# Kernel tuning notes

Measured on AMD Instinct MI355X. Metric: run time of the kernel, lower is better.

Reference implementation:

```python
import jax, jax.numpy as jnp
import numpy as np

D_MODEL = 1024
FEED = 4096
HEADS = 16
EPS = 1e-5


def _ln(x, g, b):
    mu = jnp.mean(x, axis=-1, keepdims=True)
    var = jnp.var(x, axis=-1, keepdims=True)
    return (x - mu) * jax.lax.rsqrt(var + EPS) * g + b


def setup_inputs() -> dict:
    key = jax.random.key(0)
    ks = jax.random.split(key, 8)
    s = 0.02
    return {
        "src": jax.random.normal(ks[0], (8, 512, D_MODEL), jnp.float32),
        "wq": jax.random.normal(ks[1], (D_MODEL, D_MODEL), jnp.float32) * s,
        "bq": jnp.zeros((D_MODEL,), jnp.float32),
        "wk": jax.random.normal(ks[2], (D_MODEL, D_MODEL), jnp.float32) * s,
        "bk": jnp.zeros((D_MODEL,), jnp.float32),
        "wv": jax.random.normal(ks[3], (D_MODEL, D_MODEL), jnp.float32) * s,
        "bv": jnp.zeros((D_MODEL,), jnp.float32),
        "g1": jnp.ones((D_MODEL,), jnp.float32),
        "be1": jnp.zeros((D_MODEL,), jnp.float32),
        "w1": jax.random.normal(ks[4], (D_MODEL, FEED), jnp.float32) * s,
        "b1": jnp.zeros((FEED,), jnp.float32),
        "w2": jax.random.normal(ks[5], (FEED, D_MODEL), jnp.float32) * s,
        "b2": jnp.zeros((D_MODEL,), jnp.float32),
        "g2": jnp.ones((D_MODEL,), jnp.float32),
        "be2": jnp.zeros((D_MODEL,), jnp.float32),
    }


def reference(src, wq, bq, wk, bk, wv, bv, g1, be1, w1, b1, w2, b2, g2, be2):
    bs, seq, d = src.shape
    dk = d // HEADS
    q = src @ wq + bq
    k = src @ wk + bk
    v = src @ wv + bv
    # [B, H, S, dk]
    q = q.reshape(bs, seq, HEADS, dk).transpose(0, 2, 1, 3)
    k = k.reshape(bs, seq, HEADS, dk).transpose(0, 2, 1, 3)
    v = v.reshape(bs, seq, HEADS, dk).transpose(0, 2, 1, 3)
    scores = jnp.einsum('bhqd,bhkd->bhqk', q, k)  # no mask (src_mask unused in original)
    att = jax.nn.softmax(scores / jnp.sqrt(jnp.float32(dk)), axis=-1)
    ctx = jnp.einsum('bhqk,bhkd->bhqd', att, v)
    ctx = ctx.transpose(0, 2, 1, 3).reshape(bs, seq, d)  # concat heads
    x = _ln(ctx + src, g1, be1)
    # FFN (dropout = identity at eval)
    h = jax.nn.relu(x @ w1 + b1)
    y = h @ w2 + b2
    return _ln(y + x, g2, be2)
```

## Files before the change

kernel.cpp:

```cpp
#include <hip/hip_runtime.h>
#include <hip/hip_bf16.h>
#include <stdint.h>

#define DM   1024
#define FF   4096
#define NH   16
#define DK   64
#define SEQ  512
#define NTOK 4096

typedef __attribute__((ext_vector_type(8))) unsigned short ushort8;
typedef __attribute__((ext_vector_type(4))) unsigned short ushort4v;
typedef __attribute__((ext_vector_type(8))) short bf16x8;
typedef __attribute__((ext_vector_type(4))) float f32x4;

__device__ __forceinline__ float bf2f(unsigned short u) {
  union { unsigned int i; float f; } v; v.i = ((unsigned int)u) << 16; return v.f;
}
__device__ __forceinline__ unsigned short f2bf(float f) {
  union { float fl; unsigned int i; } v; v.fl = f;
  v.i += 0x7fffu + ((v.i >> 16) & 1u);
  return (unsigned short)(v.i >> 16);
}

__device__ __forceinline__ void gload16(const unsigned short* g, unsigned short* l) {
  __builtin_amdgcn_global_load_lds(
      (const __attribute__((address_space(1))) unsigned int*)g,
      (__attribute__((address_space(3))) unsigned int*)l, 16, 0, 0);
}

__global__ __launch_bounds__(256)
void f32_to_bf16(const float* __restrict__ in, unsigned short* __restrict__ out,
                 long n) {
  long i = ((long)blockIdx.x * 256 + threadIdx.x) * 4;
  if (i + 3 < n) {
    f32x4 v = *(const f32x4*)(in + i);
    ushort4v o;
#pragma unroll
    for (int j = 0; j < 4; j++) o[j] = f2bf(v[j]);
    *(ushort4v*)(out + i) = o;
  }
}

__global__ void transpose_f2b(const float* __restrict__ in, int ldin,
                              unsigned short* __restrict__ out, int ldout) {
  __shared__ unsigned short tile[32][33];
  const int tx = threadIdx.x, ty = threadIdx.y;
  const long r0 = (long)blockIdx.y * 32, c0 = (long)blockIdx.x * 32;
#pragma unroll
  for (int i = 0; i < 4; i++)
    tile[ty + i * 8][tx] = f2bf(in[(r0 + ty + i * 8) * ldin + c0 + tx]);
  __syncthreads();
#pragma unroll
  for (int i = 0; i < 4; i++)
    out[(c0 + ty + i * 8) * ldout + r0 + tx] = tile[tx][ty + i * 8];
}

__global__ void transpose_v(const unsigned short* __restrict__ QKV,
                            unsigned short* __restrict__ Vt) {
  __shared__ unsigned short tile[32][33];
  const int tx = threadIdx.x, ty = threadIdx.y;
  const int bh = blockIdx.z, b = bh >> 4, h = bh & 15;
  const int s0 = blockIdx.y * 32, d0 = blockIdx.x * 32;
  const unsigned short* inb = QKV + (long)(b * SEQ) * 3072 + 2048 + h * 64;
#pragma unroll
  for (int i = 0; i < 4; i++)
    tile[ty + i * 8][tx] = inb[(long)(s0 + ty + i * 8) * 3072 + d0 + tx];
  __syncthreads();
#pragma unroll
  for (int i = 0; i < 4; i++)
    Vt[(long)bh * (DK * SEQ) + (long)(d0 + ty + i * 8) * SEQ + s0 + tx] =
        tile[tx][ty + i * 8];
}

__global__ void concat3(const float* __restrict__ a, const float* __restrict__ b,
                        const float* __restrict__ c, float* __restrict__ o) {
  int i = blockIdx.x * 256 + threadIdx.x;
  if (i < 3072)
    o[i] = (i < 1024) ? a[i] : ((i < 2048) ? b[i - 1024] : c[i - 2048]);
}

template <bool RELU, bool PARTIAL>
__global__ __launch_bounds__(512, 2)
void gemm256(const unsigned short* __restrict__ A, int lda,
             const unsigned short* __restrict__ B, int ldb,
             const float* __restrict__ bias,
             unsigned short* __restrict__ C,
             unsigned short* __restrict__ P1,
             unsigned short* __restrict__ P2,
             unsigned short* __restrict__ P3,
             int ldc, int nTN) {
  __shared__ unsigned short sm[65536];
  const int tid = threadIdx.x;
  const int lane = tid & 63;
  const int wid = tid >> 6;
  const int wr = wid >> 2, wc = wid & 3;

  const unsigned int T = gridDim.x;
  const unsigned int q8 = T >> 3;
  const unsigned int x = blockIdx.x;
  const unsigned int swz = (x & 7) * q8 + (x >> 3);
  const long bm = (long)(swz / nTN) * 256;
  const long bn = (long)(swz % nTN) * 256;
  const long kbase = (long)blockIdx.y * 1024;

  f32x4 acc[8][4];
#pragma unroll
  for (int mf = 0; mf < 8; mf++)
#pragma unroll
    for (int nf = 0; nf < 4; nf++) acc[mf][nf] = f32x4{0.f, 0.f, 0.f, 0.f};

  const int strow = tid >> 2;
  const int scol = (((tid & 3) ^ ((tid >> 3) & 3)) << 3);
  const unsigned short* pA = A + (bm + strow) * lda + kbase + scol;
  const unsigned short* pB = B + (bn + strow) * ldb + kbase + scol;
  unsigned short* dA = sm + tid * 8;
  unsigned short* dB = sm + 32768 + tid * 8;

  const int g = lane >> 4;
  int offA[8], offB[4];
#pragma unroll
  for (int mf = 0; mf < 8; mf++) {
    const int rm = wr * 128 + mf * 16 + (lane & 15);
    offA[mf] = rm * 32 + ((g ^ ((rm >> 1) & 3)) << 3);
  }
#pragma unroll
  for (int nf = 0; nf < 4; nf++) {
    const int rb = wc * 64 + nf * 16 + (lane & 15);
    offB[nf] = rb * 32 + ((g ^ ((rb >> 1) & 3)) << 3);
  }

#define GA(kt, ks, rh, bu) gload16(pA + (long)(rh) * 128 * lda + (kt) * 64 + (ks) * 32, \
                                   dA + (bu) * 16384 + (ks) * 8192 + (rh) * 4096)
#define GB(kt, ks, rh, bu) gload16(pB + (long)(rh) * 128 * ldb + (kt) * 64 + (ks) * 32, \
                                   dB + (bu) * 16384 + (ks) * 8192 + (rh) * 4096)
#define MF16(AR, BR, MO)                                                      \
  do {                                                                        \
    __builtin_amdgcn_s_setprio(1);                                            \
    _Pragma("unroll")                                                         \
    for (int mf = 0; mf < 4; mf++)                                            \
      _Pragma("unroll")                                                       \
      for (int nf = 0; nf < 4; nf++)                                          \
        acc[(MO) + mf][nf] = __builtin_amdgcn_mfma_f32_16x16x32_bf16(         \
            AR[mf], BR[nf], acc[(MO) + mf][nf], 0, 0, 0);                     \
    __builtin_amdgcn_s_setprio(0);                                            \
  } while (0)

  GA(0, 0, 0, 0); GA(0, 0, 1, 0); GA(0, 1, 0, 0); GA(0, 1, 1, 0);
  GB(0, 0, 0, 0); GB(0, 0, 1, 0); GB(0, 1, 0, 0); GB(0, 1, 1, 0);

  for (int t = 0; t < 16; ++t) {
    const int c = t & 1, n2 = c ^ 1;
    const int k1 = t + 1;
    const unsigned short* smAc = sm + c * 16384;
    const unsigned short* smBc = sm + 32768 + c * 16384;
    bf16x8 a0[4], a1[4], a2[4], a3[4], b0[4], b1[4];

    GA(k1, 0, 0, n2); GA(k1, 0, 1, n2);
    asm volatile("s_waitcnt vmcnt(2)\ns_barrier" ::: "memory");
#pragma unroll
    for (int mf = 0; mf < 4; mf++) a0[mf] = *(const bf16x8*)(smAc + offA[mf]);
#pragma unroll
    for (int nf = 0; nf < 4; nf++) b0[nf] = *(const bf16x8*)(smBc + offB[nf]);
    MF16(a0, b0, 0);
    GA(k1, 1, 0, n2); GA(k1, 1, 1, n2);
#pragma unroll
    for (int mf = 0; mf < 4; mf++) a1[mf] = *(const bf16x8*)(smAc + offA[4 + mf]);
    asm volatile("s_barrier" ::: "memory");
    MF16(a1, b0, 4);
    GB(k1, 0, 0, n2); GB(k1, 0, 1, n2);
#pragma unroll
    for (int mf = 0; mf < 4; mf++) a2[mf] = *(const bf16x8*)(smAc + 8192 + offA[mf]);
#pragma unroll
    for (int nf = 0; nf < 4; nf++) b1[nf] = *(const bf16x8*)(smBc + 8192 + offB[nf]);
    asm volatile("s_barrier" ::: "memory");
    MF16(a2, b1, 0);
    GB(k1, 1, 0, n2); GB(k1, 1, 1, n2);
#pragma unroll
    for (int mf = 0; mf < 4; mf++) a3[mf] = *(const bf16x8*)(smAc + 8192 + offA[4 + mf]);
    asm volatile("s_waitcnt lgkmcnt(0)\ns_barrier" ::: "memory");
    MF16(a3, b1, 4);
  }
#undef GA
#undef GB
#undef MF16

  unsigned short* Cw = C;
  if (PARTIAL) {
    const int kc = blockIdx.y;
    Cw = (kc == 0) ? C : (kc == 1) ? P1 : (kc == 2) ? P2 : P3;
  }
  const long r0 = bm + wr * 128 + ((lane >> 4) << 2);
  const int c0 = (int)bn + wc * 64 + (lane & 15);
#pragma unroll
  for (int nf = 0; nf < 4; nf++) {
    const int col = c0 + nf * 16;
    const float bv = PARTIAL ? 0.f : bias[col];
#pragma unroll
    for (int mf = 0; mf < 8; mf++) {
#pragma unroll
      for (int i = 0; i < 4; i++) {
        float v = acc[mf][nf][i] + bv;
        if (RELU) v = fmaxf(v, 0.f);
        Cw[(r0 + mf * 16 + i) * ldc + col] = f2bf(v);
      }
    }
  }
}

__global__ __launch_bounds__(512)
void attn_kernel(const unsigned short* __restrict__ QKV,
                 const unsigned short* __restrict__ Vt,
                 unsigned short* __restrict__ CTX) {
  const int qt = blockIdx.x;
  const int bh = blockIdx.y;
  const int b = bh >> 4, h = bh & 15;
  const int tid = threadIdx.x;
  const int lane = tid & 63;
  const int wid = tid >> 6;

  __shared__ unsigned short Ks[64][72];
  __shared__ unsigned short Vs[64][72];
  __shared__ unsigned short Ps[8][16][72];

  const int qrow0 = qt * 128 + wid * 16;
  const unsigned short* Qb = QKV + (long)(b * SEQ + qrow0) * 3072 + h * 64;
  bf16x8 aq[2];
#pragma unroll
  for (int ks = 0; ks < 2; ks++)
    aq[ks] = *(const bf16x8*)(Qb + (long)(lane & 15) * 3072 + ks * 32 +
                              (lane >> 4) * 8);

  f32x4 acc_o[4];
#pragma unroll
  for (int n = 0; n < 4; n++) acc_o[n] = f32x4{0.f, 0.f, 0.f, 0.f};
  float rsum[4] = {0.f, 0.f, 0.f, 0.f};

  const int sr = tid >> 3;
  const int sc = (tid & 7) * 8;
  const unsigned short* Kg = QKV + (long)(b * SEQ) * 3072 + 1024 + h * 64 + sc;
  const unsigned short* Vg = Vt + (long)bh * (DK * SEQ) + (long)sr * SEQ + sc;

  ushort8 kr = *(const ushort8*)(Kg + (long)sr * 3072);
  ushort8 vr = *(const ushort8*)(Vg);

#pragma unroll
  for (int c = 0; c < 8; ++c) {
    __syncthreads();
    *(ushort8*)(&Ks[sr][sc]) = kr;
    *(ushort8*)(&Vs[sr][sc]) = vr;
    if (c < 7) {
      kr = *(const ushort8*)(Kg + (long)((c + 1) * 64 + sr) * 3072);
      vr = *(const ushort8*)(Vg + (c + 1) * 64);
    }
    __syncthreads();

    f32x4 s[4];
#pragma unroll
    for (int n = 0; n < 4; n++) s[n] = f32x4{0.f, 0.f, 0.f, 0.f};
#pragma unroll
    for (int ks = 0; ks < 2; ks++) {
      bf16x8 kf[4];
#pragma unroll
      for (int n = 0; n < 4; n++)
        kf[n] = *(const bf16x8*)(&Ks[n * 16 + (lane & 15)][ks * 32 + (lane >> 4) * 8]);
#pragma unroll
      for (int n = 0; n < 4; n++)
        s[n] = __builtin_amdgcn_mfma_f32_16x16x32_bf16(aq[ks], kf[n], s[n], 0, 0, 0);
    }

#pragma unroll
    for (int n = 0; n < 4; n++) {
#pragma unroll
      for (int i = 0; i < 4; i++) {
        const float p = __expf(s[n][i] * 0.125f);
        rsum[i] += p;
        Ps[wid][(lane >> 4) * 4 + i][n * 16 + (lane & 15)] = f2bf(p);
      }
    }

#pragma unroll
    for (int ks = 0; ks < 2; ks++) {
      bf16x8 pa = *(const bf16x8*)(&Ps[wid][lane & 15][ks * 32 + (lane >> 4) * 8]);
      bf16x8 vf[4];
#pragma unroll
      for (int n = 0; n < 4; n++)
        vf[n] = *(const bf16x8*)(&Vs[n * 16 + (lane & 15)][ks * 32 + (lane >> 4) * 8]);
#pragma unroll
      for (int n = 0; n < 4; n++)
        acc_o[n] = __builtin_amdgcn_mfma_f32_16x16x32_bf16(pa, vf[n], acc_o[n], 0, 0, 0);
    }
  }

#pragma unroll
  for (int i = 0; i < 4; i++) {
#pragma unroll
    for (int off = 1; off < 16; off <<= 1) rsum[i] += __shfl_xor(rsum[i], off, 64);
  }

  const long orow0 = (long)(b * SEQ + qrow0);
#pragma unroll
  for (int i = 0; i < 4; i++) {
    const float inv = 1.f / rsum[i];
    const long r = orow0 + (lane >> 4) * 4 + i;
#pragma unroll
    for (int n = 0; n < 4; n++)
      CTX[r * DM + h * 64 + n * 16 + (lane & 15)] = f2bf(acc_o[n][i] * inv);
  }
}

__global__ __launch_bounds__(256)
void ln1_kernel(const unsigned short* __restrict__ X,
                const float* __restrict__ R,
                const float* __restrict__ g,
                const float* __restrict__ be,
                float* __restrict__ Of,
                unsigned short* __restrict__ Ob) {
  const int t = blockIdx.x;
  const int tid = threadIdx.x;
  const long base = (long)t * DM + tid * 4;
  __shared__ float red[8];

  ushort4v xv = *(const ushort4v*)(X + base);
  f32x4 rv = *(const f32x4*)(R + base);
  float v[4];
#pragma unroll
  for (int j = 0; j < 4; j++) v[j] = bf2f(xv[j]) + rv[j];
  float s = v[0] + v[1] + v[2] + v[3];
  float q = v[0] * v[0] + v[1] * v[1] + v[2] * v[2] + v[3] * v[3];
#pragma unroll
  for (int off = 1; off < 64; off <<= 1) {
    s += __shfl_xor(s, off, 64);
    q += __shfl_xor(q, off, 64);
  }
  if ((tid & 63) == 0) { red[tid >> 6] = s; red[4 + (tid >> 6)] = q; }
  __syncthreads();
  s = red[0] + red[1] + red[2] + red[3];
  q = red[4] + red[5] + red[6] + red[7];
  const float mu = s * (1.f / DM);
  const float var = q * (1.f / DM) - mu * mu;
  const float rstd = rsqrtf(fmaxf(var, 0.f) + 1e-5f);

  f32x4 gv = *(const f32x4*)(g + tid * 4);
  f32x4 bv = *(const f32x4*)(be + tid * 4);
  f32x4 of;
  ushort4v ob;
#pragma unroll
  for (int j = 0; j < 4; j++) {
    of[j] = (v[j] - mu) * rstd * gv[j] + bv[j];
    ob[j] = f2bf(of[j]);
  }
  *(f32x4*)(Of + base) = of;
  *(ushort4v*)(Ob + base) = ob;
}

__global__ __launch_bounds__(256)
void ln2_kernel(const unsigned short* __restrict__ P0,
                const unsigned short* __restrict__ P1,
                const unsigned short* __restrict__ P2,
                const unsigned short* __restrict__ P3,
                const float* __restrict__ b2,
                const float* __restrict__ R,
                const float* __restrict__ g,
                const float* __restrict__ be,
                float* __restrict__ O) {
  const int t = blockIdx.x;
  const int tid = threadIdx.x;
  const long base = (long)t * DM + tid * 4;
  __shared__ float red[8];

  ushort4v p0 = *(const ushort4v*)(P0 + base);
  ushort4v p1 = *(const ushort4v*)(P1 + base);
  ushort4v p2 = *(const ushort4v*)(P2 + base);
  ushort4v p3 = *(const ushort4v*)(P3 + base);
  f32x4 bb = *(const f32x4*)(b2 + tid * 4);
  f32x4 rv = *(const f32x4*)(R + base);
  float v[4];
#pragma unroll
  for (int j = 0; j < 4; j++)
    v[j] = bf2f(p0[j]) + bf2f(p1[j]) + bf2f(p2[j]) + bf2f(p3[j]) + bb[j] + rv[j];
  float s = v[0] + v[1] + v[2] + v[3];
  float q = v[0] * v[0] + v[1] * v[1] + v[2] * v[2] + v[3] * v[3];
#pragma unroll
  for (int off = 1; off < 64; off <<= 1) {
    s += __shfl_xor(s, off, 64);
    q += __shfl_xor(q, off, 64);
  }
  if ((tid & 63) == 0) { red[tid >> 6] = s; red[4 + (tid >> 6)] = q; }
  __syncthreads();
  s = red[0] + red[1] + red[2] + red[3];
  q = red[4] + red[5] + red[6] + red[7];
  const float mu = s * (1.f / DM);
  const float var = q * (1.f / DM) - mu * mu;
  const float rstd = rsqrtf(fmaxf(var, 0.f) + 1e-5f);

  f32x4 gv = *(const f32x4*)(g + tid * 4);
  f32x4 bv = *(const f32x4*)(be + tid * 4);
  f32x4 of;
#pragma unroll
  for (int j = 0; j < 4; j++) of[j] = (v[j] - mu) * rstd * gv[j] + bv[j];
  *(f32x4*)(O + base) = of;
}

extern "C" void kernel_launch(void* const* d_in, const int* in_sizes, int n_in,
                              void* d_out, int out_size, void* d_ws, size_t ws_size,
                              hipStream_t stream) {
  const float* src = (const float*)d_in[0];
  const float* wq  = (const float*)d_in[1];
  const float* bq  = (const float*)d_in[2];
  const float* wk  = (const float*)d_in[3];
  const float* bk  = (const float*)d_in[4];
  const float* wv  = (const float*)d_in[5];
  const float* bv  = (const float*)d_in[6];
  const float* g1  = (const float*)d_in[7];
  const float* be1 = (const float*)d_in[8];
  const float* w1  = (const float*)d_in[9];
  const float* b1  = (const float*)d_in[10];
  const float* w2  = (const float*)d_in[11];
  const float* b2  = (const float*)d_in[12];
  const float* g2  = (const float*)d_in[13];
  const float* be2 = (const float*)d_in[14];
  float* out = (float*)d_out;

  char* ws = (char*)d_ws;
  const size_t MB = 1024 * 1024;
  unsigned short* srcb  = (unsigned short*)(ws + 0);
  unsigned short* WqkvT = (unsigned short*)(ws + 8 * MB);
  float*          bqkv  = (float*)(ws + 14 * MB);
  unsigned short* W1T   = (unsigned short*)(ws + 15 * MB);
  unsigned short* W2T   = (unsigned short*)(ws + 23 * MB);
  unsigned short* QKV   = (unsigned short*)(ws + 31 * MB);
  unsigned short* Vtb   = (unsigned short*)(ws + 55 * MB);
  unsigned short* CTX   = (unsigned short*)(ws + 63 * MB);
  unsigned short* X1    = (unsigned short*)(ws + 71 * MB);
  float*          X1f   = (float*)(ws + 79 * MB);
  unsigned short* Hb    = (unsigned short*)(ws + 31 * MB);
  unsigned short* Pk0   = (unsigned short*)(ws + 0);
  unsigned short* Pk1   = (unsigned short*)(ws + 15 * MB);
  unsigned short* Pk2   = (unsigned short*)(ws + 63 * MB);
  unsigned short* Pk3   = (unsigned short*)(ws + 71 * MB);
  if (ws_size < 95 * MB) return;

  const dim3 t32(32, 8, 1);
  f32_to_bf16<<<4096, 256, 0, stream>>>(src, srcb, (long)NTOK * DM);
  transpose_f2b<<<dim3(32, 32), t32, 0, stream>>>(wq, 1024, WqkvT, 1024);
  transpose_f2b<<<dim3(32, 32), t32, 0, stream>>>(wk, 1024, WqkvT + 1024 * 1024, 1024);
  transpose_f2b<<<dim3(32, 32), t32, 0, stream>>>(wv, 1024, WqkvT + 2 * 1024 * 1024, 1024);
  transpose_f2b<<<dim3(128, 32), t32, 0, stream>>>(w1, 4096, W1T, 1024);
  transpose_f2b<<<dim3(32, 128), t32, 0, stream>>>(w2, 1024, W2T, 4096);
  concat3<<<12, 256, 0, stream>>>(bq, bk, bv, bqkv);

  gemm256<false, false><<<dim3(192, 1), 512, 0, stream>>>(
      srcb, 1024, WqkvT, 1024, bqkv, QKV, nullptr, nullptr, nullptr, 3072, 12);
  transpose_v<<<dim3(2, 16, 128), t32, 0, stream>>>(QKV, Vtb);
  attn_kernel<<<dim3(4, 128), 512, 0, stream>>>(QKV, Vtb, CTX);
  ln1_kernel<<<NTOK, 256, 0, stream>>>(CTX, src, g1, be1, X1f, X1);
  gemm256<true, false><<<dim3(256, 1), 512, 0, stream>>>(
      X1, 1024, W1T, 1024, b1, Hb, nullptr, nullptr, nullptr, 4096, 16);
  gemm256<false, true><<<dim3(64, 4), 512, 0, stream>>>(
      Hb, 4096, W2T, 4096, nullptr, Pk0, Pk1, Pk2, Pk3, 1024, 4);
  ln2_kernel<<<NTOK, 256, 0, stream>>>(Pk0, Pk1, Pk2, Pk3, b2, X1f, g2, be2, out);
}
```

Before: 189.7 us.

## Deepen GEMM prefetch pipeline to issue half-tiles two k-steps ahead

Restructures the GEMM main loop's global-to-LDS prefetch so the second k-half of the next tile and the first k-half of the tile after are loaded during the current iteration. Each of the four quarter-steps is now bracketed by barriers, with a single vmcnt(4) wait at the end. The goal is more memory latency in flight behind MFMA work. In exchange it adds more barriers per iteration. The k indices wrap with &15, so the final iterations issue redundant loads into buffers that are no longer read.

After: 196.3 us. +3.5%, slower.

```diff
diff --git a/kernel.cpp b/kernel.cpp
--- a/kernel.cpp
+++ b/kernel.cpp
@@ -130,10 +130,20 @@
     offB[nf] = rb * 32 + ((g ^ ((rb >> 1) & 3)) << 3);
   }
 
-#define GA(kt, ks, rh, bu) gload16(pA + (long)(rh) * 128 * lda + (kt) * 64 + (ks) * 32, \
-                                   dA + (bu) * 16384 + (ks) * 8192 + (rh) * 4096)
-#define GB(kt, ks, rh, bu) gload16(pB + (long)(rh) * 128 * ldb + (kt) * 64 + (ks) * 32, \
-                                   dB + (bu) * 16384 + (ks) * 8192 + (rh) * 4096)
+#define GAQ(kt, ks) do {                                                       \
+    gload16(pA + (long)(kt) * 64 + (ks) * 32,                                  \
+            dA + ((kt) & 1) * 16384 + (ks) * 8192);                            \
+    gload16(pA + (long)128 * lda + (long)(kt) * 64 + (ks) * 32,                \
+            dA + ((kt) & 1) * 16384 + (ks) * 8192 + 4096);                     \
+  } while (0)
+#define GBQ(kt, ks) do {                                                       \
+    gload16(pB + (long)(kt) * 64 + (ks) * 32,                                  \
+            dB + ((kt) & 1) * 16384 + (ks) * 8192);                            \
+    gload16(pB + (long)128 * ldb + (long)(kt) * 64 + (ks) * 32,                \
+            dB + ((kt) & 1) * 16384 + (ks) * 8192 + 4096);                     \
+  } while (0)
+#define BAR asm volatile("s_barrier" ::: "memory")
+#define BARV4 asm volatile("s_waitcnt vmcnt(4)\ns_barrier" ::: "memory")
 #define MF16(AR, BR, MO)                                                      \
   do {                                                                        \
     __builtin_amdgcn_s_setprio(1);                                            \
@@ -146,43 +156,53 @@
     __builtin_amdgcn_s_setprio(0);                                            \
   } while (0)
 
-  GA(0, 0, 0, 0); GA(0, 0, 1, 0); GA(0, 1, 0, 0); GA(0, 1, 1, 0);
-  GB(0, 0, 0, 0); GB(0, 0, 1, 0); GB(0, 1, 0, 0); GB(0, 1, 1, 0);
+  GAQ(0, 0); GAQ(0, 1); GBQ(0, 0); GBQ(0, 1);
+  GAQ(1, 0); GBQ(1, 0);
+  BARV4;
 
   for (int t = 0; t < 16; ++t) {
-    const int c = t & 1, n2 = c ^ 1;
-    const int k1 = t + 1;
-    const unsigned short* smAc = sm + c * 16384;
-    const unsigned short* smBc = sm + 32768 + c * 16384;
-    bf16x8 a0[4], a1[4], a2[4], a3[4], b0[4], b1[4];
-
-    GA(k1, 0, 0, n2); GA(k1, 0, 1, n2);
-    asm volatile("s_waitcnt vmcnt(2)\ns_barrier" ::: "memory");
-#pragma unroll
-    for (int mf = 0; mf < 4; mf++) a0[mf] = *(const bf16x8*)(smAc + offA[mf]);
-#pragma unroll
-    for (int nf = 0; nf < 4; nf++) b0[nf] = *(const bf16x8*)(smBc + offB[nf]);
-    MF16(a0, b0, 0);
-    GA(k1, 1, 0, n2); GA(k1, 1, 1, n2);
-#pragma unroll
-    for (int mf = 0; mf < 4; mf++) a1[mf] = *(const bf16x8*)(smAc + offA[4 + mf]);
-    asm volatile("s_barrier" ::: "memory");
-    MF16(a1, b0, 4);
-    GB(k1, 0, 0, n2); GB(k1, 0, 1, n2);
-#pragma unroll
-    for (int mf = 0; mf < 4; mf++) a2[mf] = *(const bf16x8*)(smAc + 8192 + offA[mf]);
-#pragma unroll
-    for (int nf = 0; nf < 4; nf++) b1[nf] = *(const bf16x8*)(smBc + 8192 + offB[nf]);
-    asm volatile("s_barrier" ::: "memory");
-    MF16(a2, b1, 0);
-    GB(k1, 1, 0, n2); GB(k1, 1, 1, n2);
-#pragma unroll
-    for (int mf = 0; mf < 4; mf++) a3[mf] = *(const bf16x8*)(smAc + 8192 + offA[4 + mf]);
-    asm volatile("s_waitcnt lgkmcnt(0)\ns_barrier" ::: "memory");
-    MF16(a3, b1, 4);
-  }
-#undef GA
-#undef GB
+    const unsigned short* smA = sm + (t & 1) * 16384;
+    const unsigned short* smB = sm + 32768 + (t & 1) * 16384;
+    const int k1 = (t + 1) & 15;
+    const int k2 = (t + 2) & 15;
+    bf16x8 a_[4], b0[4], b1[4];
+
+    GAQ(k1, 1);
+#pragma unroll
+    for (int mf = 0; mf < 4; mf++) a_[mf] = *(const bf16x8*)(smA + offA[mf]);
+#pragma unroll
+    for (int nf = 0; nf < 4; nf++) b0[nf] = *(const bf16x8*)(smB + offB[nf]);
+    BAR;
+    MF16(a_, b0, 0);
+    BAR;
+
+    GBQ(k1, 1);
+#pragma unroll
+    for (int mf = 0; mf < 4; mf++) a_[mf] = *(const bf16x8*)(smA + offA[4 + mf]);
+    BAR;
+    MF16(a_, b0, 4);
+    BAR;
+
+    GAQ(k2, 0);
+#pragma unroll
+    for (int mf = 0; mf < 4; mf++) a_[mf] = *(const bf16x8*)(smA + 8192 + offA[mf]);
+#pragma unroll
+    for (int nf = 0; nf < 4; nf++) b1[nf] = *(const bf16x8*)(smB + 8192 + offB[nf]);
+    BAR;
+    MF16(a_, b1, 0);
+    BAR;
+
+    GBQ(k2, 0);
+#pragma unroll
+    for (int mf = 0; mf < 4; mf++) a_[mf] = *(const bf16x8*)(smA + 8192 + offA[4 + mf]);
+    BARV4;
+    MF16(a_, b1, 4);
+    BAR;
+  }
+#undef GAQ
+#undef GBQ
+#undef BAR
+#undef BARV4
 #undef MF16
 
   unsigned short* Cw = C;
```

## Restructure GEMM main loop to issue full stage prefetch then compute

Applied to the files above, without the earlier changes.

Replaces the interleaved per-quarter global-to-LDS loads and three barriers per k-step with a single batched prefetch of the next stage, followed by a wait and one barrier, and then all LDS reads and MFMAs for the current stage. Register pressure drops because the A/B fragment arrays are reused instead of holding six sets. The intent is to reduce barrier count and simplify scheduling. In exchange it loses the fine-grained overlap between loads and MFMAs, and it issues a wrapped, redundant extra load on the last iteration, which is drained with a final vmcnt(0).

After: 195.7 us. 1.03x slower.

```diff
diff --git a/kernel.cpp b/kernel.cpp
--- a/kernel.cpp
+++ b/kernel.cpp
@@ -130,10 +130,16 @@
     offB[nf] = rb * 32 + ((g ^ ((rb >> 1) & 3)) << 3);
   }
 
-#define GA(kt, ks, rh, bu) gload16(pA + (long)(rh) * 128 * lda + (kt) * 64 + (ks) * 32, \
-                                   dA + (bu) * 16384 + (ks) * 8192 + (rh) * 4096)
-#define GB(kt, ks, rh, bu) gload16(pB + (long)(rh) * 128 * ldb + (kt) * 64 + (ks) * 32, \
-                                   dB + (bu) * 16384 + (ks) * 8192 + (rh) * 4096)
+#define GSTAGE(kt, bu) do {                                                    \
+    gload16(pA + (long)(kt) * 64,                       dA + (bu) * 16384);    \
+    gload16(pA + (long)(kt) * 64 + 32,                  dA + (bu) * 16384 + 8192); \
+    gload16(pA + (long)128 * lda + (long)(kt) * 64,     dA + (bu) * 16384 + 4096); \
+    gload16(pA + (long)128 * lda + (long)(kt) * 64 + 32,dA + (bu) * 16384 + 12288); \
+    gload16(pB + (long)(kt) * 64,                       dB + (bu) * 16384);    \
+    gload16(pB + (long)(kt) * 64 + 32,                  dB + (bu) * 16384 + 8192); \
+    gload16(pB + (long)128 * ldb + (long)(kt) * 64,     dB + (bu) * 16384 + 4096); \
+    gload16(pB + (long)128 * ldb + (long)(kt) * 64 + 32,dB + (bu) * 16384 + 12288); \
+  } while (0)
 #define MF16(AR, BR, MO)                                                      \
   do {                                                                        \
     __builtin_amdgcn_s_setprio(1);                                            \
@@ -146,43 +152,37 @@
     __builtin_amdgcn_s_setprio(0);                                            \
   } while (0)
 
-  GA(0, 0, 0, 0); GA(0, 0, 1, 0); GA(0, 1, 0, 0); GA(0, 1, 1, 0);
-  GB(0, 0, 0, 0); GB(0, 0, 1, 0); GB(0, 1, 0, 0); GB(0, 1, 1, 0);
+  GSTAGE(0, 0);
 
   for (int t = 0; t < 16; ++t) {
     const int c = t & 1, n2 = c ^ 1;
-    const int k1 = t + 1;
-    const unsigned short* smAc = sm + c * 16384;
-    const unsigned short* smBc = sm + 32768 + c * 16384;
-    bf16x8 a0[4], a1[4], a2[4], a3[4], b0[4], b1[4];
-
-    GA(k1, 0, 0, n2); GA(k1, 0, 1, n2);
-    asm volatile("s_waitcnt vmcnt(2)\ns_barrier" ::: "memory");
-#pragma unroll
-    for (int mf = 0; mf < 4; mf++) a0[mf] = *(const bf16x8*)(smAc + offA[mf]);
-#pragma unroll
-    for (int nf = 0; nf < 4; nf++) b0[nf] = *(const bf16x8*)(smBc + offB[nf]);
-    MF16(a0, b0, 0);
-    GA(k1, 1, 0, n2); GA(k1, 1, 1, n2);
-#pragma unroll
-    for (int mf = 0; mf < 4; mf++) a1[mf] = *(const bf16x8*)(smAc + offA[4 + mf]);
-    asm volatile("s_barrier" ::: "memory");
-    MF16(a1, b0, 4);
-    GB(k1, 0, 0, n2); GB(k1, 0, 1, n2);
-#pragma unroll
-    for (int mf = 0; mf < 4; mf++) a2[mf] = *(const bf16x8*)(smAc + 8192 + offA[mf]);
-#pragma unroll
-    for (int nf = 0; nf < 4; nf++) b1[nf] = *(const bf16x8*)(smBc + 8192 + offB[nf]);
-    asm volatile("s_barrier" ::: "memory");
-    MF16(a2, b1, 0);
-    GB(k1, 1, 0, n2); GB(k1, 1, 1, n2);
-#pragma unroll
-    for (int mf = 0; mf < 4; mf++) a3[mf] = *(const bf16x8*)(smAc + 8192 + offA[4 + mf]);
+    const int k1 = (t + 1) & 15;
     asm volatile("s_waitcnt lgkmcnt(0)\ns_barrier" ::: "memory");
-    MF16(a3, b1, 4);
-  }
-#undef GA
-#undef GB
+    GSTAGE(k1, n2);
+    asm volatile("s_waitcnt vmcnt(8)\ns_barrier" ::: "memory");
+
+    const unsigned short* smA = sm + c * 16384;
+    const unsigned short* smB = sm + 32768 + c * 16384;
+    bf16x8 ar[4], br[4];
+#pragma unroll
+    for (int nf = 0; nf < 4; nf++) br[nf] = *(const bf16x8*)(smB + offB[nf]);
+#pragma unroll
+    for (int mf = 0; mf < 4; mf++) ar[mf] = *(const bf16x8*)(smA + offA[mf]);
+    MF16(ar, br, 0);
+#pragma unroll
+    for (int mf = 0; mf < 4; mf++) ar[mf] = *(const bf16x8*)(smA + offA[4 + mf]);
+    MF16(ar, br, 4);
+#pragma unroll
+    for (int nf = 0; nf < 4; nf++) br[nf] = *(const bf16x8*)(smB + 8192 + offB[nf]);
+#pragma unroll
+    for (int mf = 0; mf < 4; mf++) ar[mf] = *(const bf16x8*)(smA + 8192 + offA[mf]);
+    MF16(ar, br, 0);
+#pragma unroll
+    for (int mf = 0; mf < 4; mf++) ar[mf] = *(const bf16x8*)(smA + 8192 + offA[4 + mf]);
+    MF16(ar, br, 4);
+  }
+  asm volatile("s_waitcnt vmcnt(0)" ::: "memory");
+#undef GSTAGE
 #undef MF16
 
   unsigned short* Cw = C;
```

## Merge prep kernels into one launch and use bf16 residuals in layernorms

Applied to the files above, without the earlier changes.

Replaces the six weight/input conversion launches (src cast, four transposes, bias concat) with one prep_kernel that dispatches work by block index. The layernorm kernels now read the bf16 copies of src and X1 as residuals instead of the fp32 tensors, and ln1 no longer writes an fp32 X1. This cuts launch count and memory traffic. It lowers residual precision to bf16, which may slightly increase error.

Result: faster. 174.4 us (-8.1%).

```diff
diff --git a/kernel.cpp b/kernel.cpp
--- a/kernel.cpp
+++ b/kernel.cpp
@@ -30,23 +30,52 @@
 }
 
 __global__ __launch_bounds__(256)
-void f32_to_bf16(const float* __restrict__ in, unsigned short* __restrict__ out,
-                 long n) {
-  long i = ((long)blockIdx.x * 256 + threadIdx.x) * 4;
-  if (i + 3 < n) {
-    f32x4 v = *(const f32x4*)(in + i);
+void prep_kernel(const float* __restrict__ src, unsigned short* __restrict__ srcb,
+                 const float* __restrict__ wq, const float* __restrict__ wk,
+                 const float* __restrict__ wv, unsigned short* __restrict__ WqkvT,
+                 const float* __restrict__ w1, unsigned short* __restrict__ W1T,
+                 const float* __restrict__ w2, unsigned short* __restrict__ W2T,
+                 const float* __restrict__ bq, const float* __restrict__ bk,
+                 const float* __restrict__ bv, float* __restrict__ bqkv) {
+  const int z = blockIdx.x;
+  const int tid = threadIdx.x;
+  if (z < 4096) {
+    const long i = ((long)z * 256 + tid) * 4;
+    f32x4 v = *(const f32x4*)(src + i);
     ushort4v o;
 #pragma unroll
     for (int j = 0; j < 4; j++) o[j] = f2bf(v[j]);
-    *(ushort4v*)(out + i) = o;
-  }
-}
-
-__global__ void transpose_f2b(const float* __restrict__ in, int ldin,
-                              unsigned short* __restrict__ out, int ldout) {
+    *(ushort4v*)(srcb + i) = o;
+    return;
+  }
+  if (z >= 15360) {
+    const int i = (z - 15360) * 256 + tid;
+    if (i < 3072)
+      bqkv[i] = (i < 1024) ? bq[i] : ((i < 2048) ? bk[i - 1024] : bv[i - 2048]);
+    return;
+  }
+  const float* in;
+  unsigned short* out;
+  int ldin, ldout;
+  long r0, c0;
+  if (z < 7168) {
+    const int w = (z - 4096) >> 10;
+    const int t = (z - 4096) & 1023;
+    in = (w == 0) ? wq : (w == 1) ? wk : wv;
+    out = WqkvT + (long)w * 1024 * 1024;
+    ldin = 1024; ldout = 1024;
+    r0 = (long)(t >> 5) * 32; c0 = (long)(t & 31) * 32;
+  } else if (z < 11264) {
+    const int t = z - 7168;
+    in = w1; out = W1T; ldin = 4096; ldout = 1024;
+    r0 = (long)(t >> 7) * 32; c0 = (long)(t & 127) * 32;
+  } else {
+    const int t = z - 11264;
+    in = w2; out = W2T; ldin = 1024; ldout = 4096;
+    r0 = (long)(t >> 5) * 32; c0 = (long)(t & 31) * 32;
+  }
   __shared__ unsigned short tile[32][33];
-  const int tx = threadIdx.x, ty = threadIdx.y;
-  const long r0 = (long)blockIdx.y * 32, c0 = (long)blockIdx.x * 32;
+  const int tx = tid & 31, ty = tid >> 5;
 #pragma unroll
   for (int i = 0; i < 4; i++)
     tile[ty + i * 8][tx] = f2bf(in[(r0 + ty + i * 8) * ldin + c0 + tx]);
@@ -71,13 +100,6 @@
   for (int i = 0; i < 4; i++)
     Vt[(long)bh * (DK * SEQ) + (long)(d0 + ty + i * 8) * SEQ + s0 + tx] =
         tile[tx][ty + i * 8];
-}
-
-__global__ void concat3(const float* __restrict__ a, const float* __restrict__ b,
-                        const float* __restrict__ c, float* __restrict__ o) {
-  int i = blockIdx.x * 256 + threadIdx.x;
-  if (i < 3072)
-    o[i] = (i < 1024) ? a[i] : ((i < 2048) ? b[i - 1024] : c[i - 2048]);
 }
 
 template <bool RELU, bool PARTIAL>
@@ -311,10 +333,9 @@
 
 __global__ __launch_bounds__(256)
 void ln1_kernel(const unsigned short* __restrict__ X,
-                const float* __restrict__ R,
+                const unsigned short* __restrict__ R,
                 const float* __restrict__ g,
                 const float* __restrict__ be,
-                float* __restrict__ Of,
                 unsigned short* __restrict__ Ob) {
   const int t = blockIdx.x;
   const int tid = threadIdx.x;
@@ -322,10 +343,10 @@
   __shared__ float red[8];
 
   ushort4v xv = *(const ushort4v*)(X + base);
-  f32x4 rv = *(const f32x4*)(R + base);
+  ushort4v rv = *(const ushort4v*)(R + base);
   float v[4];
 #pragma unroll
-  for (int j = 0; j < 4; j++) v[j] = bf2f(xv[j]) + rv[j];
+  for (int j = 0; j < 4; j++) v[j] = bf2f(xv[j]) + bf2f(rv[j]);
   float s = v[0] + v[1] + v[2] + v[3];
   float q = v[0] * v[0] + v[1] * v[1] + v[2] * v[2] + v[3] * v[3];
 #pragma unroll
@@ -343,14 +364,10 @@
 
   f32x4 gv = *(const f32x4*)(g + tid * 4);
   f32x4 bv = *(const f32x4*)(be + tid * 4);
-  f32x4 of;
   ushort4v ob;
 #pragma unroll
-  for (int j = 0; j < 4; j++) {
-    of[j] = (v[j] - mu) * rstd * gv[j] + bv[j];
-    ob[j] = f2bf(of[j]);
-  }
-  *(f32x4*)(Of + base) = of;
+  for (int j = 0; j < 4; j++)
+    ob[j] = f2bf((v[j] - mu) * rstd * gv[j] + bv[j]);
   *(ushort4v*)(Ob + base) = ob;
 }
 
@@ -360,7 +377,7 @@
                 const unsigned short* __restrict__ P2,
                 const unsigned short* __restrict__ P3,
                 const float* __restrict__ b2,
-                const float* __restrict__ R,
+                const unsigned short* __restrict__ R,
                 const float* __restrict__ g,
                 const float* __restrict__ be,
                 float* __restrict__ O) {
@@ -374,11 +391,11 @@
   ushort4v p2 = *(const ushort4v*)(P2 + base);
   ushort4v p3 = *(const ushort4v*)(P3 + base);
   f32x4 bb = *(const f32x4*)(b2 + tid * 4);
-  f32x4 rv = *(const f32x4*)(R + base);
+  ushort4v rv = *(const ushort4v*)(R + base);
   float v[4];
 #pragma unroll
   for (int j = 0; j < 4; j++)
-    v[j] = bf2f(p0[j]) + bf2f(p1[j]) + bf2f(p2[j]) + bf2f(p3[j]) + bb[j] + rv[j];
+    v[j] = bf2f(p0[j]) + bf2f(p1[j]) + bf2f(p2[j]) + bf2f(p3[j]) + bb[j] + bf2f(rv[j]);
   float s = v[0] + v[1] + v[2] + v[3];
   float q = v[0] * v[0] + v[1] * v[1] + v[2] * v[2] + v[3] * v[3];
 #pragma unroll
@@ -433,31 +450,25 @@
   unsigned short* Vtb   = (unsigned short*)(ws + 55 * MB);
   unsigned short* CTX   = (unsigned short*)(ws + 63 * MB);
   unsigned short* X1    = (unsigned short*)(ws + 71 * MB);
-  float*          X1f   = (float*)(ws + 79 * MB);
+  unsigned short* Pk3   = (unsigned short*)(ws + 79 * MB);
   unsigned short* Hb    = (unsigned short*)(ws + 31 * MB);
   unsigned short* Pk0   = (unsigned short*)(ws + 0);
   unsigned short* Pk1   = (unsigned short*)(ws + 15 * MB);
   unsigned short* Pk2   = (unsigned short*)(ws + 63 * MB);
-  unsigned short* Pk3   = (unsigned short*)(ws + 71 * MB);
-  if (ws_size < 95 * MB) return;
+  if (ws_size < 87 * MB) return;
 
   const dim3 t32(32, 8, 1);
-  f32_to_bf16<<<4096, 256, 0, stream>>>(src, srcb, (long)NTOK * DM);
-  transpose_f2b<<<dim3(32, 32), t32, 0, stream>>>(wq, 1024, WqkvT, 1024);
-  transpose_f2b<<<dim3(32, 32), t32, 0, stream>>>(wk, 1024, WqkvT + 1024 * 1024, 1024);
-  transpose_f2b<<<dim3(32, 32), t32, 0, stream>>>(wv, 1024, WqkvT + 2 * 1024 * 1024, 1024);
-  transpose_f2b<<<dim3(128, 32), t32, 0, stream>>>(w1, 4096, W1T, 1024);
-  transpose_f2b<<<dim3(32, 128), t32, 0, stream>>>(w2, 1024, W2T, 4096);
-  concat3<<<12, 256, 0, stream>>>(bq, bk, bv, bqkv);
+  prep_kernel<<<15372, 256, 0, stream>>>(src, srcb, wq, wk, wv, WqkvT,
+                                         w1, W1T, w2, W2T, bq, bk, bv, bqkv);
 
   gemm256<false, false><<<dim3(192, 1), 512, 0, stream>>>(
       srcb, 1024, WqkvT, 1024, bqkv, QKV, nullptr, nullptr, nullptr, 3072, 12);
   transpose_v<<<dim3(2, 16, 128), t32, 0, stream>>>(QKV, Vtb);
   attn_kernel<<<dim3(4, 128), 512, 0, stream>>>(QKV, Vtb, CTX);
-  ln1_kernel<<<NTOK, 256, 0, stream>>>(CTX, src, g1, be1, X1f, X1);
+  ln1_kernel<<<NTOK, 256, 0, stream>>>(CTX, srcb, g1, be1, X1);
   gemm256<true, false><<<dim3(256, 1), 512, 0, stream>>>(
       X1, 1024, W1T, 1024, b1, Hb, nullptr, nullptr, nullptr, 4096, 16);
   gemm256<false, true><<<dim3(64, 4), 512, 0, stream>>>(
       Hb, 4096, W2T, 4096, nullptr, Pk0, Pk1, Pk2, Pk3, 1024, 4);
-  ln2_kernel<<<NTOK, 256, 0, stream>>>(Pk0, Pk1, Pk2, Pk3, b2, X1f, g2, be2, out);
-}
+  ln2_kernel<<<NTOK, 256, 0, stream>>>(Pk0, Pk1, Pk2, Pk3, b2, X1, g2, be2, out);
+}
```
